# Performance work log

Measured on AMD Instinct MI355X. Metric: run time of the kernel, lower is better.

The kernel has to match this reference:

```python
import jax, jax.numpy as jnp
import numpy as np

LN_EPS = 1e-5  # torch LayerNorm default
K_NN = 5       # top-5 nearest patterns (simple-surprise path)


def setup_inputs() -> dict:
    key = jax.random.key(0)
    ks = jax.random.split(key, 5)
    B, S, D, M = 8, 8192, 256, 50
    return {
        "hidden_states": jax.random.normal(ks[0], (B, S, D), dtype=jnp.float32),
        "memory": jax.random.normal(ks[1], (M, D), dtype=jnp.float32),
        "W1": jax.random.normal(ks[2], (D, 2 * D), dtype=jnp.float32) * (1.0 / np.sqrt(D)),
        "b1": jnp.zeros((2 * D,), dtype=jnp.float32),
        "W2": jax.random.normal(ks[3], (2 * D, D), dtype=jnp.float32) * (1.0 / np.sqrt(2 * D)),
        "b2": jnp.zeros((D,), dtype=jnp.float32),
        "ln_gamma": jnp.ones((D,), dtype=jnp.float32),
        "ln_beta": jnp.zeros((D,), dtype=jnp.float32),
    }


def reference(hidden_states, memory, W1, b1, W2, b2, ln_gamma, ln_beta):
    # Feature extractor: Linear -> ReLU -> (Dropout, eval=identity) -> Linear -> LayerNorm
    h = jax.nn.relu(jnp.einsum("bsd,de->bse", hidden_states, W1) + b1)
    f = jnp.einsum("bse,ed->bsd", h, W2) + b2
    mu = jnp.mean(f, axis=-1, keepdims=True)
    var = jnp.var(f, axis=-1, keepdims=True)
    feats = (f - mu) * jax.lax.rsqrt(var + LN_EPS) * ln_gamma + ln_beta  # [B,S,D]

    # Simple-surprise path, vectorized over all (b, s) tokens:
    # L2 distance of each token feature to every memory pattern.
    f_sq = jnp.sum(feats * feats, axis=-1)      # [B,S]
    m_sq = jnp.sum(memory * memory, axis=-1)    # [M]
    dots = jnp.einsum("bsd,md->bsm", feats, memory)  # [B,S,M]
    d2 = jnp.maximum(f_sq[..., None] + m_sq - 2.0 * dots, 0.0)
    dists = jnp.sqrt(d2)                        # [B,S,M]

    # k smallest distances -> mean -> sigmoid(avg - 1)
    neg_knn, _ = jax.lax.top_k(-dists, K_NN)    # [B,S,K]
    avg_dist = -jnp.mean(neg_knn, axis=-1)      # [B,S]
    surprise_scores = jax.nn.sigmoid(avg_dist - 1.0)
    return surprise_scores
```

## Files before the change

### kernel.cpp

```cpp
#include <hip/hip_runtime.h>
#include <math.h>

typedef __attribute__((ext_vector_type(8))) short bf16x8;
typedef __attribute__((ext_vector_type(4))) float f32x4;

static __device__ __forceinline__ unsigned short f2b(float x) {
  unsigned int u = __float_as_uint(x);
  u += 0x7FFFu + ((u >> 16) & 1u);
  return (unsigned short)(u >> 16);
}

static __device__ __forceinline__ unsigned int cvtpk(float lo, float hi) {
  unsigned int r;
  asm("v_cvt_pk_bf16_f32 %0, %1, %2" : "=v"(r) : "v"(lo), "v"(hi));
  return r;
}

__global__ void prep_weights(const float* __restrict__ W1,
                             const float* __restrict__ W2,
                             const float* __restrict__ mem,
                             unsigned short* __restrict__ W1T,
                             unsigned short* __restrict__ W2T,
                             unsigned short* __restrict__ memB,
                             float* __restrict__ msq) {
  int i = blockIdx.x * 256 + threadIdx.x;
  if (i < 131072) {
    int k = i >> 9, n = i & 511;
    W1T[n * 256 + k] = f2b(W1[i]);
  } else if (i < 262144) {
    int j = i - 131072;
    int k = j >> 8, n = j & 255;
    W2T[n * 512 + k] = f2b(W2[j]);
  } else if (i < 278528) {
    int j = i - 262144;
    int r = j >> 8;
    memB[j] = (r < 50) ? f2b(mem[j]) : (unsigned short)0;
  } else {
    int t = threadIdx.x;
    int r = t >> 2, c0 = (t & 3) * 64;
    float s = 0.f;
    if (r < 50) {
      for (int c = 0; c < 64; ++c) {
        float v = mem[r * 256 + c0 + c];
        s += v * v;
      }
    }
    s += __shfl_xor(s, 1, 64);
    s += __shfl_xor(s, 2, 64);
    if ((t & 3) == 0) msq[r] = (r < 50) ? s : 1e30f;
  }
}

#define DPitch 53
#define SWZ(b, r) ((b) ^ (((r) & 7) << 4))

__global__ __launch_bounds__(256, 2) void fused_main(
    const float* __restrict__ X, const float* __restrict__ b1v,
    const float* __restrict__ b2v, const float* __restrict__ gammav,
    const float* __restrict__ betav, const unsigned short* __restrict__ W1T,
    const unsigned short* __restrict__ W2T,
    const unsigned short* __restrict__ memB, const float* __restrict__ msq,
    float* __restrict__ out) {
  __shared__ __align__(16) char smem[65536];
  float* distS = (float*)smem;
  float* red = (float*)(smem + 32768);
  float* psum   = red;
  float* psumsq = red + 256;
  float* fsqp   = red + 512;
  float* muS    = red + 768;
  float* rstdS  = red + 832;
  float* fsqS   = red + 896;

  const char* W1Tc = (const char*)W1T;
  const char* W2Tc = (const char*)W2T;

  const int tid = threadIdx.x;
  const int wid = tid >> 6;
  const int lane = tid & 63;
  const int l16 = lane & 15;
  const int quad = lane >> 4;

  const float4* X4 = (const float4*)(X + (size_t)blockIdx.x * 64 * 256);
#pragma unroll
  for (int j = 0; j < 16; ++j) {
    int row = j * 4 + wid;
    float4 v = X4[row * 64 + lane];
    *(uint2*)(smem + SWZ(row * 512 + lane * 8, row)) =
        make_uint2(cvtpk(v.x, v.y), cvtpk(v.z, v.w));
  }

  f32x4 acc2[4][4];
#pragma unroll
  for (int mt = 0; mt < 4; ++mt) {
    const float4 bb = *(const float4*)(&b2v[wid * 64 + mt * 16 + quad * 4]);
#pragma unroll
    for (int nt = 0; nt < 4; ++nt) {
      acc2[mt][nt][0] = bb.x; acc2[mt][nt][1] = bb.y;
      acc2[mt][nt][2] = bb.z; acc2[mt][nt][3] = bb.w;
    }
  }

  __syncthreads();

#pragma unroll
  for (int cc = 0; cc < 4; ++cc) {
    if (cc > 0) {
      const char* HsR = smem + 32768 + ((cc - 1) & 1) * 16384;
#pragma unroll
      for (int k2 = 0; k2 < 4; ++k2) {
        bf16x8 a[4], b[4];
#pragma unroll
        for (int mt = 0; mt < 4; ++mt)
          a[mt] = *(const bf16x8*)(W2Tc + (wid * 64 + mt * 16 + l16) * 1024 +
                                   (cc - 1) * 256 + k2 * 64 + quad * 16);
#pragma unroll
        for (int nt = 0; nt < 4; ++nt) {
          int r = nt * 16 + l16;
          b[nt] = *(const bf16x8*)(HsR + SWZ(r * 256 + k2 * 64 + quad * 16, r));
        }
#pragma unroll
        for (int mt = 0; mt < 4; ++mt)
#pragma unroll
          for (int nt = 0; nt < 4; ++nt)
            acc2[mt][nt] = __builtin_amdgcn_mfma_f32_16x16x32_bf16(
                a[mt], b[nt], acc2[mt][nt], 0, 0, 0);
      }
    }

    int hbase = cc * 128 + wid * 32;
    f32x4 acc1[2][4];
#pragma unroll
    for (int mt = 0; mt < 2; ++mt) {
      const float4 bb = *(const float4*)(&b1v[hbase + mt * 16 + quad * 4]);
#pragma unroll
      for (int nt = 0; nt < 4; ++nt) {
        acc1[mt][nt][0] = bb.x; acc1[mt][nt][1] = bb.y;
        acc1[mt][nt][2] = bb.z; acc1[mt][nt][3] = bb.w;
      }
    }
#pragma unroll
    for (int kk = 0; kk < 8; ++kk) {
      int kb = kk * 64 + quad * 16;
      bf16x8 a[2], b[4];
#pragma unroll
      for (int mt = 0; mt < 2; ++mt)
        a[mt] = *(const bf16x8*)(W1Tc + (hbase + mt * 16 + l16) * 512 + kb);
#pragma unroll
      for (int nt = 0; nt < 4; ++nt) {
        int r = nt * 16 + l16;
        b[nt] = *(const bf16x8*)(smem + SWZ(r * 512 + kb, r));
      }
#pragma unroll
      for (int mt = 0; mt < 2; ++mt)
#pragma unroll
        for (int nt = 0; nt < 4; ++nt)
          acc1[mt][nt] = __builtin_amdgcn_mfma_f32_16x16x32_bf16(
              a[mt], b[nt], acc1[mt][nt], 0, 0, 0);
    }
    {
      char* HsW = smem + 32768 + (cc & 1) * 16384;
#pragma unroll
      for (int mt = 0; mt < 2; ++mt)
#pragma unroll
        for (int nt = 0; nt < 4; ++nt) {
          int token = nt * 16 + l16;
          f32x4 v = acc1[mt][nt];
          *(uint2*)(HsW + SWZ(token * 256 + wid * 64 + mt * 32 + quad * 8, token)) =
              make_uint2(cvtpk(fmaxf(v[0], 0.f), fmaxf(v[1], 0.f)),
                         cvtpk(fmaxf(v[2], 0.f), fmaxf(v[3], 0.f)));
        }
    }
    __syncthreads();
  }

  {
    const char* HsR = smem + 32768 + 16384;
#pragma unroll
    for (int k2 = 0; k2 < 4; ++k2) {
      bf16x8 a[4], b[4];
#pragma unroll
      for (int mt = 0; mt < 4; ++mt)
        a[mt] = *(const bf16x8*)(W2Tc + (wid * 64 + mt * 16 + l16) * 1024 +
                                 3 * 256 + k2 * 64 + quad * 16);
#pragma unroll
      for (int nt = 0; nt < 4; ++nt) {
        int r = nt * 16 + l16;
        b[nt] = *(const bf16x8*)(HsR + SWZ(r * 256 + k2 * 64 + quad * 16, r));
      }
#pragma unroll
      for (int mt = 0; mt < 4; ++mt)
#pragma unroll
        for (int nt = 0; nt < 4; ++nt)
          acc2[mt][nt] = __builtin_amdgcn_mfma_f32_16x16x32_bf16(
              a[mt], b[nt], acc2[mt][nt], 0, 0, 0);
    }
  }

#pragma unroll
  for (int nt = 0; nt < 4; ++nt) {
    float s = 0.f, sq = 0.f;
#pragma unroll
    for (int mt = 0; mt < 4; ++mt)
#pragma unroll
      for (int r = 0; r < 4; ++r) {
        float v = acc2[mt][nt][r];
        s += v; sq += v * v;
      }
    s += __shfl_xor(s, 16, 64); sq += __shfl_xor(sq, 16, 64);
    s += __shfl_xor(s, 32, 64); sq += __shfl_xor(sq, 32, 64);
    if (quad == 0) {
      psum[wid * 64 + nt * 16 + l16] = s;
      psumsq[wid * 64 + nt * 16 + l16] = sq;
    }
  }
  __syncthreads();
  if (tid < 64) {
    float s = psum[tid] + psum[64 + tid] + psum[128 + tid] + psum[192 + tid];
    float sq = psumsq[tid] + psumsq[64 + tid] + psumsq[128 + tid] + psumsq[192 + tid];
    float mu = s * (1.f / 256.f);
    float var = sq * (1.f / 256.f) - mu * mu;
    muS[tid] = mu;
    rstdS[tid] = rsqrtf(var + 1e-5f);
  }
  __syncthreads();

  {
    float4 g[4], be[4];
#pragma unroll
    for (int mt = 0; mt < 4; ++mt) {
      g[mt]  = *(const float4*)(&gammav[wid * 64 + mt * 16 + quad * 4]);
      be[mt] = *(const float4*)(&betav[wid * 64 + mt * 16 + quad * 4]);
    }
#pragma unroll
    for (int nt = 0; nt < 4; ++nt) {
      int token = nt * 16 + l16;
      float mu = muS[token], rs = rstdS[token];
      float fs = 0.f;
#pragma unroll
      for (int mt = 0; mt < 4; ++mt) {
        float y0 = (acc2[mt][nt][0] - mu) * rs * g[mt].x + be[mt].x;
        float y1 = (acc2[mt][nt][1] - mu) * rs * g[mt].y + be[mt].y;
        float y2 = (acc2[mt][nt][2] - mu) * rs * g[mt].z + be[mt].z;
        float y3 = (acc2[mt][nt][3] - mu) * rs * g[mt].w + be[mt].w;
        fs += y0 * y0 + y1 * y1 + y2 * y2 + y3 * y3;
        *(uint2*)(smem + SWZ(token * 512 + wid * 128 + mt * 32 + quad * 8, token)) =
            make_uint2(cvtpk(y0, y1), cvtpk(y2, y3));
      }
      fs += __shfl_xor(fs, 16, 64);
      fs += __shfl_xor(fs, 32, 64);
      if (quad == 0) fsqp[wid * 64 + token] = fs;
    }
  }
  __syncthreads();
  if (tid < 64)
    fsqS[tid] = fsqp[tid] + fsqp[64 + tid] + fsqp[128 + tid] + fsqp[192 + tid];
  __syncthreads();

  f32x4 acc3[4];
#pragma unroll
  for (int nt = 0; nt < 4; ++nt) {
    acc3[nt][0] = 0.f; acc3[nt][1] = 0.f; acc3[nt][2] = 0.f; acc3[nt][3] = 0.f;
  }
#pragma unroll
  for (int kk = 0; kk < 8; ++kk) {
    int kb = kk * 64 + quad * 16;
    int ar = wid * 16 + l16;
    bf16x8 a = *(const bf16x8*)(smem + SWZ(ar * 512 + kb, ar));
    int k0 = kk * 32 + quad * 8;
#pragma unroll
    for (int nt = 0; nt < 4; ++nt) {
      bf16x8 b = *(const bf16x8*)(memB + (nt * 16 + l16) * 256 + k0);
      acc3[nt] = __builtin_amdgcn_mfma_f32_16x16x32_bf16(a, b, acc3[nt], 0, 0, 0);
    }
  }
  __syncthreads();
  {
    float4 fsq4 = *(const float4*)(&fsqS[wid * 16 + quad * 4]);
#pragma unroll
    for (int nt = 0; nt < 4; ++nt) {
      int col = nt * 16 + l16;
      float mq = msq[col];
#pragma unroll
      for (int r = 0; r < 4; ++r) {
        float fv = (r == 0) ? fsq4.x : (r == 1) ? fsq4.y : (r == 2) ? fsq4.z : fsq4.w;
        float d2 = fv + mq - 2.f * acc3[nt][r];
        float d = sqrtf(fmaxf(d2, 0.f));
        int row = wid * 16 + quad * 4 + r;
        if (col < 50) distS[row * DPitch + col] = d;
      }
    }
  }
  __syncthreads();

  if (tid < 64) {
    float b0 = 1e30f, b1 = 1e30f, b2 = 1e30f, b3 = 1e30f, b4 = 1e30f;
    const float* dr = &distS[tid * DPitch];
    for (int j = 0; j < 50; ++j) {
      float v = dr[j];
      b4 = fminf(b4, v);
      float t;
      if (b4 < b3) { t = b3; b3 = b4; b4 = t; }
      if (b3 < b2) { t = b2; b2 = b3; b3 = t; }
      if (b2 < b1) { t = b1; b1 = b2; b2 = t; }
      if (b1 < b0) { t = b0; b0 = b1; b1 = t; }
    }
    float avg = (b0 + b1 + b2 + b3 + b4) * 0.2f;
    float sarg = avg - 1.f;
    out[blockIdx.x * 64 + tid] = 1.f / (1.f + __expf(-sarg));
  }
}

extern "C" void kernel_launch(void* const* d_in, const int* in_sizes, int n_in,
                              void* d_out, int out_size, void* d_ws, size_t ws_size,
                              hipStream_t stream) {
  const float* X   = (const float*)d_in[0];
  const float* mem = (const float*)d_in[1];
  const float* W1  = (const float*)d_in[2];
  const float* b1  = (const float*)d_in[3];
  const float* W2  = (const float*)d_in[4];
  const float* b2  = (const float*)d_in[5];
  const float* g   = (const float*)d_in[6];
  const float* be  = (const float*)d_in[7];
  float* out = (float*)d_out;

  unsigned short* W1T  = (unsigned short*)d_ws;
  unsigned short* W2T  = W1T + 131072;
  unsigned short* memB = W2T + 131072;
  float* msq = (float*)(memB + 16384);

  prep_weights<<<1089, 256, 0, stream>>>(W1, W2, mem, W1T, W2T, memB, msq);
  fused_main<<<1024, 256, 0, stream>>>(X, b1, b2, g, be, W1T, W2T, memB, msq, out);
}
```

Before: 189.3 us.

## Use 8 waves per block in fused kernel and tile weight-prep transposes

```diff
diff --git a/kernel.cpp b/kernel.cpp
--- a/kernel.cpp
+++ b/kernel.cpp
@@ -3,12 +3,6 @@
 
 typedef __attribute__((ext_vector_type(8))) short bf16x8;
 typedef __attribute__((ext_vector_type(4))) float f32x4;
-
-static __device__ __forceinline__ unsigned short f2b(float x) {
-  unsigned int u = __float_as_uint(x);
-  u += 0x7FFFu + ((u >> 16) & 1u);
-  return (unsigned short)(u >> 16);
-}
 
 static __device__ __forceinline__ unsigned int cvtpk(float lo, float hi) {
   unsigned int r;
@@ -23,38 +17,75 @@
                              unsigned short* __restrict__ W2T,
                              unsigned short* __restrict__ memB,
                              float* __restrict__ msq) {
-  int i = blockIdx.x * 256 + threadIdx.x;
-  if (i < 131072) {
-    int k = i >> 9, n = i & 511;
-    W1T[n * 256 + k] = f2b(W1[i]);
-  } else if (i < 262144) {
-    int j = i - 131072;
-    int k = j >> 8, n = j & 255;
-    W2T[n * 512 + k] = f2b(W2[j]);
-  } else if (i < 278528) {
-    int j = i - 262144;
-    int r = j >> 8;
-    memB[j] = (r < 50) ? f2b(mem[j]) : (unsigned short)0;
+  const int bid = blockIdx.x, tid = threadIdx.x;
+  if (bid < 64) {
+    __shared__ float tile[64][65];
+    const float* src;
+    unsigned short* dst;
+    int C, Cd, k0, n0;
+    if (bid < 32) {
+      src = W1; dst = W1T; C = 512; Cd = 256;
+      k0 = (bid >> 3) * 64; n0 = (bid & 7) * 64;
+    } else {
+      int t = bid - 32;
+      src = W2; dst = W2T; C = 256; Cd = 512;
+      k0 = (t >> 2) * 64; n0 = (t & 3) * 64;
+    }
+    int r = tid >> 2, c4 = (tid & 3) * 16;
+    const float4* s4 = (const float4*)(src + (k0 + r) * C + n0 + c4);
+#pragma unroll
+    for (int j = 0; j < 4; ++j) {
+      float4 v = s4[j];
+      tile[r][c4 + j * 4 + 0] = v.x;
+      tile[r][c4 + j * 4 + 1] = v.y;
+      tile[r][c4 + j * 4 + 2] = v.z;
+      tile[r][c4 + j * 4 + 3] = v.w;
+    }
+    __syncthreads();
+    int nl = tid >> 2, kq = (tid & 3) * 16;
+    unsigned int o[8];
+#pragma unroll
+    for (int j = 0; j < 8; ++j)
+      o[j] = cvtpk(tile[kq + 2 * j][nl], tile[kq + 2 * j + 1][nl]);
+    unsigned short* dp = dst + (n0 + nl) * Cd + k0 + kq;
+    *(uint4*)(dp) = make_uint4(o[0], o[1], o[2], o[3]);
+    *(uint4*)(dp + 8) = make_uint4(o[4], o[5], o[6], o[7]);
+  } else if (bid == 64) {
+    int j0 = tid * 64;
+#pragma unroll
+    for (int j = 0; j < 16; ++j) {
+      int e = j0 + j * 4;
+      int rrow = e >> 8;
+      uint2 w;
+      if (rrow < 50) {
+        float4 v = *(const float4*)(mem + e);
+        w = make_uint2(cvtpk(v.x, v.y), cvtpk(v.z, v.w));
+      } else {
+        w = make_uint2(0u, 0u);
+      }
+      *(uint2*)(memB + e) = w;
+    }
   } else {
-    int t = threadIdx.x;
-    int r = t >> 2, c0 = (t & 3) * 64;
+    int rrow = tid >> 2, c0 = (tid & 3) * 64;
     float s = 0.f;
-    if (r < 50) {
-      for (int c = 0; c < 64; ++c) {
-        float v = mem[r * 256 + c0 + c];
-        s += v * v;
+    if (rrow < 50) {
+      const float4* m4 = (const float4*)(mem + rrow * 256 + c0);
+#pragma unroll
+      for (int c = 0; c < 16; ++c) {
+        float4 v = m4[c];
+        s += v.x * v.x + v.y * v.y + v.z * v.z + v.w * v.w;
       }
     }
     s += __shfl_xor(s, 1, 64);
     s += __shfl_xor(s, 2, 64);
-    if ((t & 3) == 0) msq[r] = (r < 50) ? s : 1e30f;
+    if ((tid & 3) == 0) msq[rrow] = (rrow < 50) ? s : 1e30f;
   }
 }
 
 #define DPitch 53
 #define SWZ(b, r) ((b) ^ (((r) & 7) << 4))
 
-__global__ __launch_bounds__(256, 2) void fused_main(
+__global__ __launch_bounds__(512, 4) void fused_main(
     const float* __restrict__ X, const float* __restrict__ b1v,
     const float* __restrict__ b2v, const float* __restrict__ gammav,
     const float* __restrict__ betav, const unsigned short* __restrict__ W1T,
@@ -65,11 +96,11 @@
   float* distS = (float*)smem;
   float* red = (float*)(smem + 32768);
   float* psum   = red;
-  float* psumsq = red + 256;
-  float* fsqp   = red + 512;
-  float* muS    = red + 768;
-  float* rstdS  = red + 832;
-  float* fsqS   = red + 896;
+  float* psumsq = red + 512;
+  float* fsqp   = red + 1024;
+  float* muS    = red + 1536;
+  float* rstdS  = red + 1600;
+  float* fsqS   = red + 1664;
 
   const char* W1Tc = (const char*)W1T;
   const char* W2Tc = (const char*)W2T;
@@ -82,17 +113,17 @@
 
   const float4* X4 = (const float4*)(X + (size_t)blockIdx.x * 64 * 256);
 #pragma unroll
-  for (int j = 0; j < 16; ++j) {
-    int row = j * 4 + wid;
+  for (int j = 0; j < 8; ++j) {
+    int row = j * 8 + wid;
     float4 v = X4[row * 64 + lane];
     *(uint2*)(smem + SWZ(row * 512 + lane * 8, row)) =
         make_uint2(cvtpk(v.x, v.y), cvtpk(v.z, v.w));
   }
 
-  f32x4 acc2[4][4];
-#pragma unroll
-  for (int mt = 0; mt < 4; ++mt) {
-    const float4 bb = *(const float4*)(&b2v[wid * 64 + mt * 16 + quad * 4]);
+  f32x4 acc2[2][4];
+#pragma unroll
+  for (int mt = 0; mt < 2; ++mt) {
+    const float4 bb = *(const float4*)(&b2v[wid * 32 + mt * 16 + quad * 4]);
 #pragma unroll
     for (int nt = 0; nt < 4; ++nt) {
       acc2[mt][nt][0] = bb.x; acc2[mt][nt][1] = bb.y;
@@ -108,10 +139,10 @@
       const char* HsR = smem + 32768 + ((cc - 1) & 1) * 16384;
 #pragma unroll
       for (int k2 = 0; k2 < 4; ++k2) {
-        bf16x8 a[4], b[4];
-#pragma unroll
-        for (int mt = 0; mt < 4; ++mt)
-          a[mt] = *(const bf16x8*)(W2Tc + (wid * 64 + mt * 16 + l16) * 1024 +
+        bf16x8 a[2], b[4];
+#pragma unroll
+        for (int mt = 0; mt < 2; ++mt)
+          a[mt] = *(const bf16x8*)(W2Tc + (wid * 32 + mt * 16 + l16) * 1024 +
                                    (cc - 1) * 256 + k2 * 64 + quad * 16);
 #pragma unroll
         for (int nt = 0; nt < 4; ++nt) {
@@ -119,7 +150,7 @@
           b[nt] = *(const bf16x8*)(HsR + SWZ(r * 256 + k2 * 64 + quad * 16, r));
         }
 #pragma unroll
-        for (int mt = 0; mt < 4; ++mt)
+        for (int mt = 0; mt < 2; ++mt)
 #pragma unroll
           for (int nt = 0; nt < 4; ++nt)
             acc2[mt][nt] = __builtin_amdgcn_mfma_f32_16x16x32_bf16(
@@ -127,48 +158,40 @@
       }
     }
 
-    int hbase = cc * 128 + wid * 32;
-    f32x4 acc1[2][4];
-#pragma unroll
-    for (int mt = 0; mt < 2; ++mt) {
-      const float4 bb = *(const float4*)(&b1v[hbase + mt * 16 + quad * 4]);
+    int hbase = cc * 128 + wid * 16;
+    f32x4 acc1[4];
+    {
+      const float4 bb = *(const float4*)(&b1v[hbase + quad * 4]);
 #pragma unroll
       for (int nt = 0; nt < 4; ++nt) {
-        acc1[mt][nt][0] = bb.x; acc1[mt][nt][1] = bb.y;
-        acc1[mt][nt][2] = bb.z; acc1[mt][nt][3] = bb.w;
+        acc1[nt][0] = bb.x; acc1[nt][1] = bb.y;
+        acc1[nt][2] = bb.z; acc1[nt][3] = bb.w;
       }
     }
 #pragma unroll
     for (int kk = 0; kk < 8; ++kk) {
       int kb = kk * 64 + quad * 16;
-      bf16x8 a[2], b[4];
-#pragma unroll
-      for (int mt = 0; mt < 2; ++mt)
-        a[mt] = *(const bf16x8*)(W1Tc + (hbase + mt * 16 + l16) * 512 + kb);
+      bf16x8 a = *(const bf16x8*)(W1Tc + (hbase + l16) * 512 + kb);
+      bf16x8 b[4];
 #pragma unroll
       for (int nt = 0; nt < 4; ++nt) {
         int r = nt * 16 + l16;
         b[nt] = *(const bf16x8*)(smem + SWZ(r * 512 + kb, r));
       }
 #pragma unroll
-      for (int mt = 0; mt < 2; ++mt)
-#pragma unroll
-        for (int nt = 0; nt < 4; ++nt)
-          acc1[mt][nt] = __builtin_amdgcn_mfma_f32_16x16x32_bf16(
-              a[mt], b[nt], acc1[mt][nt], 0, 0, 0);
+      for (int nt = 0; nt < 4; ++nt)
+        acc1[nt] = __builtin_amdgcn_mfma_f32_16x16x32_bf16(a, b[nt], acc1[nt], 0, 0, 0);
     }
     {
       char* HsW = smem + 32768 + (cc & 1) * 16384;
 #pragma unroll
-      for (int mt = 0; mt < 2; ++mt)
-#pragma unroll
-        for (int nt = 0; nt < 4; ++nt) {
-          int token = nt * 16 + l16;
-          f32x4 v = acc1[mt][nt];
-          *(uint2*)(HsW + SWZ(token * 256 + wid * 64 + mt * 32 + quad * 8, token)) =
-              make_uint2(cvtpk(fmaxf(v[0], 0.f), fmaxf(v[1], 0.f)),
-                         cvtpk(fmaxf(v[2], 0.f), fmaxf(v[3], 0.f)));
-        }
+      for (int nt = 0; nt < 4; ++nt) {
+        int token = nt * 16 + l16;
+        f32x4 v = acc1[nt];
+        *(uint2*)(HsW + SWZ(token * 256 + wid * 32 + quad * 8, token)) =
+            make_uint2(cvtpk(fmaxf(v[0], 0.f), fmaxf(v[1], 0.f)),
+                       cvtpk(fmaxf(v[2], 0.f), fmaxf(v[3], 0.f)));
+      }
     }
     __syncthreads();
   }
@@ -177,10 +200,10 @@
     const char* HsR = smem + 32768 + 16384;
 #pragma unroll
     for (int k2 = 0; k2 < 4; ++k2) {
-      bf16x8 a[4], b[4];
-#pragma unroll
-      for (int mt = 0; mt < 4; ++mt)
-        a[mt] = *(const bf16x8*)(W2Tc + (wid * 64 + mt * 16 + l16) * 1024 +
+      bf16x8 a[2], b[4];
+#pragma unroll
+      for (int mt = 0; mt < 2; ++mt)
+        a[mt] = *(const bf16x8*)(W2Tc + (wid * 32 + mt * 16 + l16) * 1024 +
                                  3 * 256 + k2 * 64 + quad * 16);
 #pragma unroll
       for (int nt = 0; nt < 4; ++nt) {
@@ -188,7 +211,7 @@
         b[nt] = *(const bf16x8*)(HsR + SWZ(r * 256 + k2 * 64 + quad * 16, r));
       }
 #pragma unroll
-      for (int mt = 0; mt < 4; ++mt)
+      for (int mt = 0; mt < 2; ++mt)
 #pragma unroll
         for (int nt = 0; nt < 4; ++nt)
           acc2[mt][nt] = __builtin_amdgcn_mfma_f32_16x16x32_bf16(
@@ -200,7 +223,7 @@
   for (int nt = 0; nt < 4; ++nt) {
     float s = 0.f, sq = 0.f;
 #pragma unroll
-    for (int mt = 0; mt < 4; ++mt)
+    for (int mt = 0; mt < 2; ++mt)
 #pragma unroll
       for (int r = 0; r < 4; ++r) {
         float v = acc2[mt][nt][r];
@@ -215,8 +238,12 @@
   }
   __syncthreads();
   if (tid < 64) {
-    float s = psum[tid] + psum[64 + tid] + psum[128 + tid] + psum[192 + tid];
-    float sq = psumsq[tid] + psumsq[64 + tid] + psumsq[128 + tid] + psumsq[192 + tid];
+    float s = 0.f, sq = 0.f;
+#pragma unroll
+    for (int w = 0; w < 8; ++w) {
+      s += psum[w * 64 + tid];
+      sq += psumsq[w * 64 + tid];
+    }
     float mu = s * (1.f / 256.f);
     float var = sq * (1.f / 256.f) - mu * mu;
     muS[tid] = mu;
@@ -225,11 +252,11 @@
   __syncthreads();
 
   {
-    float4 g[4], be[4];
-#pragma unroll
-    for (int mt = 0; mt < 4; ++mt) {
-      g[mt]  = *(const float4*)(&gammav[wid * 64 + mt * 16 + quad * 4]);
-      be[mt] = *(const float4*)(&betav[wid * 64 + mt * 16 + quad * 4]);
+    float4 g[2], be_[2];
+#pragma unroll
+    for (int mt = 0; mt < 2; ++mt) {
+      g[mt]   = *(const float4*)(&gammav[wid * 32 + mt * 16 + quad * 4]);
+      be_[mt] = *(const float4*)(&betav[wid * 32 + mt * 16 + quad * 4]);
     }
 #pragma unroll
     for (int nt = 0; nt < 4; ++nt) {
@@ -237,13 +264,13 @@
       float mu = muS[token], rs = rstdS[token];
       float fs = 0.f;
 #pragma unroll
-      for (int mt = 0; mt < 4; ++mt) {
-        float y0 = (acc2[mt][nt][0] - mu) * rs * g[mt].x + be[mt].x;
-        float y1 = (acc2[mt][nt][1] - mu) * rs * g[mt].y + be[mt].y;
-        float y2 = (acc2[mt][nt][2] - mu) * rs * g[mt].z + be[mt].z;
-        float y3 = (acc2[mt][nt][3] - mu) * rs * g[mt].w + be[mt].w;
+      for (int mt = 0; mt < 2; ++mt) {
+        float y0 = (acc2[mt][nt][0] - mu) * rs * g[mt].x + be_[mt].x;
+        float y1 = (acc2[mt][nt][1] - mu) * rs * g[mt].y + be_[mt].y;
+        float y2 = (acc2[mt][nt][2] - mu) * rs * g[mt].z + be_[mt].z;
+        float y3 = (acc2[mt][nt][3] - mu) * rs * g[mt].w + be_[mt].w;
         fs += y0 * y0 + y1 * y1 + y2 * y2 + y3 * y3;
-        *(uint2*)(smem + SWZ(token * 512 + wid * 128 + mt * 32 + quad * 8, token)) =
+        *(uint2*)(smem + SWZ(token * 512 + wid * 64 + mt * 32 + quad * 8, token)) =
             make_uint2(cvtpk(y0, y1), cvtpk(y2, y3));
       }
       fs += __shfl_xor(fs, 16, 64);
@@ -252,40 +279,45 @@
     }
   }
   __syncthreads();
-  if (tid < 64)
-    fsqS[tid] = fsqp[tid] + fsqp[64 + tid] + fsqp[128 + tid] + fsqp[192 + tid];
-  __syncthreads();
-
-  f32x4 acc3[4];
-#pragma unroll
-  for (int nt = 0; nt < 4; ++nt) {
-    acc3[nt][0] = 0.f; acc3[nt][1] = 0.f; acc3[nt][2] = 0.f; acc3[nt][3] = 0.f;
-  }
-#pragma unroll
-  for (int kk = 0; kk < 8; ++kk) {
-    int kb = kk * 64 + quad * 16;
-    int ar = wid * 16 + l16;
-    bf16x8 a = *(const bf16x8*)(smem + SWZ(ar * 512 + kb, ar));
-    int k0 = kk * 32 + quad * 8;
-#pragma unroll
-    for (int nt = 0; nt < 4; ++nt) {
-      bf16x8 b = *(const bf16x8*)(memB + (nt * 16 + l16) * 256 + k0);
-      acc3[nt] = __builtin_amdgcn_mfma_f32_16x16x32_bf16(a, b, acc3[nt], 0, 0, 0);
-    }
-  }
-  __syncthreads();
+  if (tid < 64) {
+    float fs = 0.f;
+#pragma unroll
+    for (int w = 0; w < 8; ++w) fs += fsqp[w * 64 + tid];
+    fsqS[tid] = fs;
+  }
+  __syncthreads();
+
   {
-    float4 fsq4 = *(const float4*)(&fsqS[wid * 16 + quad * 4]);
-#pragma unroll
-    for (int nt = 0; nt < 4; ++nt) {
-      int col = nt * 16 + l16;
+    const int th = wid & 3, mh = wid >> 2;
+    f32x4 acc3[2];
+#pragma unroll
+    for (int j = 0; j < 2; ++j) {
+      acc3[j][0] = 0.f; acc3[j][1] = 0.f; acc3[j][2] = 0.f; acc3[j][3] = 0.f;
+    }
+    const int ar = th * 16 + l16;
+#pragma unroll
+    for (int kk = 0; kk < 8; ++kk) {
+      int kb = kk * 64 + quad * 16;
+      bf16x8 a = *(const bf16x8*)(smem + SWZ(ar * 512 + kb, ar));
+      int k0 = kk * 32 + quad * 8;
+#pragma unroll
+      for (int j = 0; j < 2; ++j) {
+        bf16x8 b = *(const bf16x8*)(memB + (mh * 32 + j * 16 + l16) * 256 + k0);
+        acc3[j] = __builtin_amdgcn_mfma_f32_16x16x32_bf16(a, b, acc3[j], 0, 0, 0);
+      }
+    }
+    __syncthreads();
+    float4 fsq4 = *(const float4*)(&fsqS[th * 16 + quad * 4]);
+#pragma unroll
+    for (int j = 0; j < 2; ++j) {
+      int col = mh * 32 + j * 16 + l16;
       float mq = msq[col];
 #pragma unroll
       for (int r = 0; r < 4; ++r) {
         float fv = (r == 0) ? fsq4.x : (r == 1) ? fsq4.y : (r == 2) ? fsq4.z : fsq4.w;
-        float d2 = fv + mq - 2.f * acc3[nt][r];
+        float d2 = fv + mq - 2.f * acc3[j][r];
         float d = sqrtf(fmaxf(d2, 0.f));
-        int row = wid * 16 + quad * 4 + r;
+        int row = th * 16 + quad * 4 + r;
         if (col < 50) distS[row * DPitch + col] = d;
       }
     }
@@ -328,6 +360,6 @@
   unsigned short* memB = W2T + 131072;
   float* msq = (float*)(memB + 16384);
 
-  prep_weights<<<1089, 256, 0, stream>>>(W1, W2, mem, W1T, W2T, memB, msq);
-  fused_main<<<1024, 256, 0, stream>>>(X, b1, b2, g, be, W1T, W2T, memB, msq, out);
+  prep_weights<<<66, 256, 0, stream>>>(W1, W2, mem, W1T, W2T, memB, msq);
+  fused_main<<<1024, 512, 0, stream>>>(X, b1, b2, g, be, W1T, W2T, memB, msq, out);
 }
```

New measurement: 194.2 us. 1.03x slower.
